# Kernel optimization log

Measured on AMD Instinct MI355X. Metric: run time of the kernel, lower is better.

The kernel has to match this reference:

```python
import jax, jax.numpy as jnp
import numpy as np

N = 50000   # nodes
E = 800000  # edges
H = 4       # num_heads
D = 32      # out_dim
IN = 256    # in_dim


def setup_inputs() -> dict:
    key = jax.random.key(0)
    k0, k1, k2, k3, k4, k5 = jax.random.split(key, 6)
    h = jax.random.normal(k0, (N, IN), dtype=jnp.float32)
    # fl weight (torch Linear stores [out, in]), xavier-ish scale
    Wl = jax.random.normal(k1, (H * D, IN), dtype=jnp.float32) * (1.0 / np.sqrt(IN))
    # fc / fq are initialized to small constants in torch; use small random here
    fc = jax.random.normal(k2, (IN, H * D), dtype=jnp.float32) * 0.02
    fq = jax.random.normal(k3, (IN, H * D), dtype=jnp.float32) * 0.02
    src = jax.random.randint(k4, (E,), 0, N)
    dst = jax.random.randint(k5, (E,), 0, N)
    return {"h": h, "Wl": Wl, "fc": fc, "fq": fq, "src": src, "dst": dst}


def reference(h, Wl, fc, fq, src, dst):
    n = h.shape[0]
    ft = (h @ Wl.T).reshape(n, H, D)      # [N,H,D]
    ft_c = (h @ fc).reshape(n, H, D)      # [N,H,D]
    ft_q = (h @ fq).reshape(n, H, D)      # [N,H,D]

    # edge attention: c = ft_c[dst], q = ft_q[src] - c, a = ELU(sum(q*c))
    c = ft_c[dst]                         # [E,H,D]
    a = jax.nn.elu(jnp.sum((ft_q[src] - c) * c, axis=-1))  # [E,H]

    # segmented (per-destination) softmax over incoming edges, per head
    m = jax.ops.segment_max(a, dst, num_segments=n)        # [N,H]
    ex = jnp.exp(a - m[dst])
    s = jax.ops.segment_sum(ex, dst, num_segments=n)       # [N,H]
    attn = ex / s[dst]                                     # [E,H]

    # global top-k (smallest l_s) threshold + mass redistribution, per head
    l_s = int(0.713 * attn.shape[0])
    srt = jnp.sort(attn, axis=0)                           # ascending per head
    thd = srt[l_s - 1]                                     # [H] l_s-th smallest
    topk_sum = jnp.sum(srt[:l_s], axis=0)                  # [H]
    a2 = jnp.where(attn - thd < 0, jnp.zeros((), attn.dtype), attn)
    ratio = (jnp.sum(a2, axis=0) + topk_sum) / jnp.sum(a2, axis=0)  # [H]
    a3 = a2 * ratio                                        # [E,H]

    # weighted scatter-sum of source features to destinations
    out = jax.ops.segment_sum(ft[src] * a3[:, :, None], dst, num_segments=n)  # [N,H,D]

    # concat=True: cat(flattened heads, mean over heads of ft)
    return jnp.concatenate([out.reshape(n, -1), ft.mean(axis=1)], axis=1)  # [N, H*D + D]
```

## Files before the change

kernel.cpp:

```cpp
#include <hip/hip_runtime.h>
#include <hip/hip_bf16.h>
#include <math.h>

#define N_NODES 50000
#define N_EDGES 800000
#define NH 4
#define DH 32
#define IN_DIM 256
#define OUTC 160
#define LS 570400
#define RANK0 (LS - 1)
#define DEG_CAP 160

typedef unsigned long long u64;
#define SC_FX 1099511627776.0

__global__ void k_deg(const int* __restrict__ dst, unsigned* __restrict__ A){
  int e = blockIdx.x * 256 + threadIdx.x;
  if (e < N_EDGES) atomicAdd(&A[dst[e]], 1u);
}

__global__ __launch_bounds__(1024) void k_scan(unsigned* __restrict__ A){
  __shared__ unsigned ps[1024];
  int t = threadIdx.x;
  const int CH = (N_NODES + 1023) / 1024;
  int base = t * CH;
  unsigned s = 0;
  for (int i = 0; i < CH; i++){ int n = base + i; if (n < N_NODES) s += A[n]; }
  ps[t] = s;
  __syncthreads();
  for (int off = 1; off < 1024; off <<= 1){
    unsigned v = (t >= off) ? ps[t - off] : 0;
    __syncthreads();
    ps[t] += v;
    __syncthreads();
  }
  unsigned ex = (t == 0) ? 0 : ps[t - 1];
  for (int i = 0; i < CH; i++){
    int n = base + i;
    if (n < N_NODES){ unsigned dv = A[n]; A[n] = ex; ex += dv; }
  }
}

__global__ void k_fill(const int* __restrict__ dst, unsigned* __restrict__ A,
                       unsigned* __restrict__ eidx){
  int e = blockIdx.x * 256 + threadIdx.x;
  if (e < N_EDGES) eidx[atomicAdd(&A[dst[e]], 1u)] = (unsigned)e;
}

__global__ void k_init(u64* __restrict__ sel4, unsigned* __restrict__ krem,
                       unsigned* __restrict__ cnt, unsigned* __restrict__ done,
                       unsigned* __restrict__ ccnt, u64* __restrict__ gsums){
  int t = threadIdx.x;
  if (t < 4){ sel4[t] = 0; krem[t] = RANK0; cnt[t] = 0; ccnt[t] = 0; }
  if (t < 8) gsums[t] = 0;
  if (t == 0) done[0] = 0;
}

#define BM 128
#define BK 16
__global__ __launch_bounds__(256) void k_gemm32(const float* __restrict__ A,
                                                const float* __restrict__ Wl,
                                                float* __restrict__ C){
  __shared__ float As[BK][BM + 4];
  __shared__ float Bs[BK][128 + 4];
  int tid = threadIdx.x;
  int m0 = blockIdx.x * BM;
  int ty = tid / 16, tx = tid % 16;
  float acc[8][8];
  #pragma unroll
  for (int i = 0; i < 8; i++)
    #pragma unroll
    for (int j = 0; j < 8; j++) acc[i][j] = 0.f;

  for (int k0 = 0; k0 < IN_DIM; k0 += BK){
    #pragma unroll
    for (int i = 0; i < 2; i++){
      int s = tid * 2 + i;
      int row = s >> 2, c4 = s & 3;
      int r = m0 + row;
      float4 v = make_float4(0.f, 0.f, 0.f, 0.f);
      if (r < N_NODES) v = *(const float4*)&A[(size_t)r * IN_DIM + k0 + c4 * 4];
      As[c4 * 4 + 0][row] = v.x; As[c4 * 4 + 1][row] = v.y;
      As[c4 * 4 + 2][row] = v.z; As[c4 * 4 + 3][row] = v.w;
    }
    #pragma unroll
    for (int i = 0; i < 2; i++){
      int s = tid * 2 + i;
      int j = s >> 2, c4 = s & 3;
      float4 v = *(const float4*)&Wl[(size_t)j * IN_DIM + k0 + c4 * 4];
      Bs[c4 * 4 + 0][j] = v.x; Bs[c4 * 4 + 1][j] = v.y;
      Bs[c4 * 4 + 2][j] = v.z; Bs[c4 * 4 + 3][j] = v.w;
    }
    __syncthreads();
    #pragma unroll
    for (int kk = 0; kk < BK; kk++){
      float4 a0 = *(const float4*)&As[kk][ty * 4];
      float4 a1 = *(const float4*)&As[kk][64 + ty * 4];
      float4 b0 = *(const float4*)&Bs[kk][tx * 4];
      float4 b1 = *(const float4*)&Bs[kk][64 + tx * 4];
      float av[8] = {a0.x, a0.y, a0.z, a0.w, a1.x, a1.y, a1.z, a1.w};
      float bv[8] = {b0.x, b0.y, b0.z, b0.w, b1.x, b1.y, b1.z, b1.w};
      #pragma unroll
      for (int i = 0; i < 8; i++)
        #pragma unroll
        for (int j = 0; j < 8; j++)
          acc[i][j] = fmaf(av[i], bv[j], acc[i][j]);
    }
    __syncthreads();
  }
  #pragma unroll
  for (int i = 0; i < 8; i++){
    int r = m0 + ((i < 4) ? (ty * 4 + i) : (64 + ty * 4 + (i - 4)));
    if (r >= N_NODES) continue;
    *(float4*)&C[(size_t)r * 128 + tx * 4]      = make_float4(acc[i][0], acc[i][1], acc[i][2], acc[i][3]);
    *(float4*)&C[(size_t)r * 128 + 64 + tx * 4] = make_float4(acc[i][4], acc[i][5], acc[i][6], acc[i][7]);
  }
}

__global__ __launch_bounds__(256) void k_gemm64(const float* __restrict__ A,
                                                const float* __restrict__ fc,
                                                const float* __restrict__ fq,
                                                double* __restrict__ c64,
                                                double* __restrict__ q64){
  __shared__ double As[16][66];
  __shared__ double Bs[16][66];
  int tid = threadIdx.x;
  int m0 = blockIdx.x * 64;
  int n0 = blockIdx.y * 64;
  const float* Bsrc = (n0 < 128) ? fc : fq;
  int j0 = (n0 < 128) ? n0 : n0 - 128;
  double* Cp = (n0 < 128) ? c64 : q64;
  int ty = tid / 16, tx = tid % 16;
  double acc[4][4];
  #pragma unroll
  for (int i = 0; i < 4; i++)
    #pragma unroll
    for (int j = 0; j < 4; j++) acc[i][j] = 0.0;

  for (int k0 = 0; k0 < IN_DIM; k0 += 16){
    {
      int row = tid >> 2, c4 = tid & 3;
      int r = m0 + row;
      float4 v = make_float4(0.f, 0.f, 0.f, 0.f);
      if (r < N_NODES) v = *(const float4*)&A[(size_t)r * IN_DIM + k0 + c4 * 4];
      As[c4 * 4 + 0][row] = (double)v.x; As[c4 * 4 + 1][row] = (double)v.y;
      As[c4 * 4 + 2][row] = (double)v.z; As[c4 * 4 + 3][row] = (double)v.w;
    }
    {
      int kr = tid >> 4, c4 = tid & 15;
      float4 v = *(const float4*)&Bsrc[(size_t)(k0 + kr) * 128 + j0 + c4 * 4];
      Bs[kr][c4 * 4 + 0] = (double)v.x; Bs[kr][c4 * 4 + 1] = (double)v.y;
      Bs[kr][c4 * 4 + 2] = (double)v.z; Bs[kr][c4 * 4 + 3] = (double)v.w;
    }
    __syncthreads();
    #pragma unroll
    for (int kk = 0; kk < 16; kk++){
      double a[4], b[4];
      #pragma unroll
      for (int i = 0; i < 4; i++) a[i] = As[kk][ty * 4 + i];
      #pragma unroll
      for (int j = 0; j < 4; j++) b[j] = Bs[kk][tx + 16 * j];
      #pragma unroll
      for (int i = 0; i < 4; i++)
        #pragma unroll
        for (int j = 0; j < 4; j++)
          acc[i][j] = fma(a[i], b[j], acc[i][j]);
    }
    __syncthreads();
  }
  #pragma unroll
  for (int i = 0; i < 4; i++){
    int r = m0 + ty * 4 + i;
    if (r >= N_NODES) continue;
    double* p = &Cp[(size_t)r * 128 + j0];
    #pragma unroll
    for (int j = 0; j < 4; j++) p[tx + 16 * j] = acc[i][j];
  }
}

__global__ __launch_bounds__(256) void k_softedge(const double* __restrict__ c64,
    const double* __restrict__ q64, const int* __restrict__ src,
    const unsigned* __restrict__ A, const unsigned* __restrict__ eidx,
    double* __restrict__ abuf){
  __shared__ double lds_a[4][DEG_CAP * 4];
  int d = blockIdx.x * 4 + (threadIdx.x >> 6);
  int t = threadIdx.x & 63;
  int wv = threadIdx.x >> 6;
  if (d >= N_NODES) return;
  unsigned k0 = d ? A[d - 1] : 0u, k1 = A[d];
  if (k0 == k1) return;
  double2 c = *(const double2*)&c64[(size_t)d * 128 + t * 2];
  double m = -1.0e300;
  int sn = src[eidx[k0]];
  double2 qn = *(const double2*)&q64[(size_t)sn * 128 + t * 2];
  for (unsigned k = k0; k < k1; k++){
    double2 q = qn;
    if (k + 1 < k1){
      int s2 = src[eidx[k + 1]];
      qn = *(const double2*)&q64[(size_t)s2 * 128 + t * 2];
    }
    double val = (q.x - c.x) * c.x + (q.y - c.y) * c.y;
    val += __shfl_xor(val, 1);
    val += __shfl_xor(val, 2);
    val += __shfl_xor(val, 4);
    val += __shfl_xor(val, 8);
    double a = (val > 0.0) ? val : expm1(val);
    m = fmax(m, a);
    if ((t & 15) == 0) lds_a[wv][(k - k0) * 4 + (t >> 4)] = a;
  }
  double mm = __shfl(m, (t & 3) * 16);
  unsigned nj = (k1 - k0) * 4;
  long long sfx = 0;
  for (unsigned jj = t; jj < nj; jj += 64){
    double ex = exp(lds_a[wv][jj] - mm);
    lds_a[wv][jj] = ex;
    sfx += llrint(ex * SC_FX);
  }
  #pragma unroll
  for (int msk = 4; msk < 64; msk <<= 1) sfx += __shfl_xor(sfx, msk);
  double sd = (double)sfx * (1.0 / SC_FX);
  for (unsigned jj = t; jj < nj; jj += 64)
    abuf[(size_t)k0 * 4 + jj] = lds_a[wv][jj] / sd;
}

__global__ __launch_bounds__(256) void k_hp(const double* __restrict__ attn,
    u64* __restrict__ sel4, unsigned* __restrict__ krem, unsigned* __restrict__ cnt,
    unsigned* __restrict__ hist, unsigned* __restrict__ done, u64 maskHi, int shift){
  __shared__ unsigned lh[1024];
  __shared__ unsigned ticket;
  for (int j = threadIdx.x; j < 1024; j += 256) lh[j] = 0;
  __syncthreads();
  int i0 = blockIdx.x * 256 + threadIdx.x;
  int hh = i0 & 3;
  u64 sel = sel4[hh] & maskHi;
  const int total = N_EDGES * 4;
  for (int i = i0; i < total; i += gridDim.x * 256){
    u64 u = (u64)__double_as_longlong(attn[i]);
    if ((u & maskHi) == sel)
      atomicAdd(&lh[hh * 256 + (unsigned)((u >> shift) & 255u)], 1u);
  }
  __syncthreads();
  for (int j = threadIdx.x; j < 1024; j += 256)
    if (lh[j]) atomicAdd(&hist[j], lh[j]);
  __threadfence();
  if (threadIdx.x == 0) ticket = atomicAdd(done, 1u);
  __syncthreads();
  if (ticket == gridDim.x - 1){
    __threadfence();
    for (int j = threadIdx.x; j < 1024; j += 256){ lh[j] = hist[j]; hist[j] = 0; }
    __syncthreads();
    if (threadIdx.x < 4){
      int t = threadIdx.x;
      unsigned kr = krem[t], cum = 0, b = 0;
      for (; b < 256; b++){
        unsigned c2 = lh[t * 256 + b];
        if (kr < cum + c2) break;
        cum += c2;
      }
      sel4[t] |= ((u64)b) << shift;
      krem[t] = kr - cum;
      cnt[t] += cum;
    }
    if (threadIdx.x == 0) *done = 0;
  }
}

__global__ __launch_bounds__(256) void k_compact(const double* __restrict__ attn,
    const u64* __restrict__ sel4, unsigned* __restrict__ ccnt,
    double* __restrict__ cand){
  __shared__ unsigned lcnt[4];
  __shared__ unsigned lbase[4];
  int t = threadIdx.x;
  if (t < 4) lcnt[t] = 0;
  __syncthreads();
  int i0 = blockIdx.x * 256 + t;
  int hh = i0 & 3;
  u64 sel = sel4[hh] & 0xFFFF000000000000ull;
  const int total = N_EDGES * 4;
  unsigned mc = 0;
  for (int i = i0; i < total; i += gridDim.x * 256){
    u64 u = (u64)__double_as_longlong(attn[i]);
    if ((u & 0xFFFF000000000000ull) == sel) mc++;
  }
  unsigned my_local = mc ? atomicAdd(&lcnt[hh], mc) : 0u;
  __syncthreads();
  if (t < 4) lbase[t] = lcnt[t] ? atomicAdd(&ccnt[t], lcnt[t]) : 0u;
  __syncthreads();
  if (mc == 0) return;
  unsigned pos = lbase[hh] + my_local;
  double* cp = cand + (size_t)hh * N_EDGES;
  for (int i = i0; i < total; i += gridDim.x * 256){
    double v = attn[i];
    u64 u = (u64)__double_as_longlong(v);
    if ((u & 0xFFFF000000000000ull) == sel) cp[pos++] = v;
  }
}

__global__ __launch_bounds__(256) void k_fin2(const double* __restrict__ cand,
    const unsigned* __restrict__ ccnt, u64* __restrict__ sel4,
    unsigned* __restrict__ krem, unsigned* __restrict__ cnt,
    unsigned* __restrict__ hist, unsigned* __restrict__ done, int shift){
  __shared__ unsigned lh[256];
  __shared__ unsigned ticket;
  int t = threadIdx.x;
  lh[t] = 0;
  __syncthreads();
  int h = blockIdx.x & 3;
  int bidx = blockIdx.x >> 2;
  int bph = gridDim.x >> 2;
  u64 maskHi = ~((1ull << (shift + 8)) - 1);
  u64 sel = sel4[h] & maskHi;
  unsigned n = ccnt[h];
  const double* cp = cand + (size_t)h * N_EDGES;
  for (unsigned i = bidx * 256 + t; i < n; i += bph * 256){
    u64 u = (u64)__double_as_longlong(cp[i]);
    if ((u & maskHi) == sel) atomicAdd(&lh[(unsigned)((u >> shift) & 255u)], 1u);
  }
  __syncthreads();
  if (lh[t]) atomicAdd(&hist[h * 256 + t], lh[t]);
  __threadfence();
  if (t == 0) ticket = atomicAdd(done, 1u);
  __syncthreads();
  if (ticket == gridDim.x - 1){
    __threadfence();
    __shared__ unsigned fh[1024];
    for (int j = t; j < 1024; j += 256){ fh[j] = hist[j]; hist[j] = 0; }
    __syncthreads();
    if (t < 4){
      unsigned kr = krem[t], cum = 0, b = 0;
      for (; b < 256; b++){
        unsigned c2 = fh[t * 256 + b];
        if (kr < cum + c2) break;
        cum += c2;
      }
      sel4[t] |= ((u64)b) << shift;
      krem[t] = kr - cum;
      cnt[t] += cum;
    }
    if (t == 0) *done = 0;
  }
}

__global__ __launch_bounds__(256) void k_sums(const double* __restrict__ attn,
    const u64* __restrict__ sel4, u64* __restrict__ gsums, float* __restrict__ a3){
  int t = threadIdx.x;
  int i0 = blockIdx.x * 256 + t;
  int hh = t & 3;
  double thd = __longlong_as_double((long long)sel4[hh]);
  double al = 0.0, ag = 0.0;
  const int total = N_EDGES * 4;
  for (int i = i0; i < total; i += gridDim.x * 256){
    double v = attn[i];
    if (v < thd){ al += v; a3[i] = 0.f; }
    else        { ag += v; a3[i] = (float)v; }
  }
  long long ql = llrint(al * SC_FX);
  long long qg = llrint(ag * SC_FX);
  #pragma unroll
  for (int m = 4; m < 64; m <<= 1){
    ql += __shfl_xor(ql, m);
    qg += __shfl_xor(qg, m);
  }
  __shared__ long long sl[16], sg[16];
  int wv = t >> 6;
  if ((t & 63) < 4){ sl[wv * 4 + hh] = ql; sg[wv * 4 + hh] = qg; }
  __syncthreads();
  if (t < 4){
    long long a = sl[t] + sl[4 + t] + sl[8 + t] + sl[12 + t];
    long long b = sg[t] + sg[4 + t] + sg[8 + t] + sg[12 + t];
    if (a) atomicAdd(&gsums[t],     (u64)a);
    if (b) atomicAdd(&gsums[4 + t], (u64)b);
  }
}

__global__ void k_ratio(const u64* __restrict__ sel4, const unsigned* __restrict__ cnt,
                        const u64* __restrict__ gsums, double* __restrict__ trd){
  int t = threadIdx.x;
  if (t < 4){
    double thd = __longlong_as_double((long long)sel4[t]);
    double sless = (double)gsums[t]     * (1.0 / SC_FX);
    double sge   = (double)gsums[4 + t] * (1.0 / SC_FX);
    double topk  = sless + (double)(LS - (int)cnt[t]) * thd;
    trd[t] = thd;
    trd[4 + t] = (sge + topk) / sge;
  }
}

__global__ __launch_bounds__(256) void k_scatter2(const float* __restrict__ ft,
    const int* __restrict__ src, const unsigned* __restrict__ A,
    const unsigned* __restrict__ eidx, const float* __restrict__ a3,
    const double* __restrict__ trd, float* __restrict__ out){
  int d = blockIdx.x * 4 + (threadIdx.x >> 6);
  int t = threadIdx.x & 63;
  if (d >= N_NODES) return;
  int hh = t >> 4;
  double ratio = trd[4 + hh];
  unsigned k0 = d ? A[d - 1] : 0u, k1 = A[d];
  long long acc0 = 0, acc1 = 0;
  float wn = (k0 < k1) ? a3[(size_t)k0 * 4 + hh] : 0.f;
  unsigned en = (k0 < k1) ? eidx[k0] : 0u;
  for (unsigned k = k0; k < k1; k++){
    float w = wn;
    unsigned e = en;
    if (k + 1 < k1){ wn = a3[(size_t)(k + 1) * 4 + hh]; en = eidx[k + 1]; }
    if (__ballot(w != 0.f) == 0ull) continue;
    if (w != 0.f){
      int s = src[e];
      float2 f = *(const float2*)&ft[(size_t)s * 128 + t * 2];
      double a3r = (double)w * ratio;
      acc0 += llrint(a3r * (double)f.x * SC_FX);
      acc1 += llrint(a3r * (double)f.y * SC_FX);
    }
  }
  float* p = &out[(size_t)d * OUTC + t * 2];
  p[0] = (float)((double)acc0 * (1.0 / SC_FX));
  p[1] = (float)((double)acc1 * (1.0 / SC_FX));
}

__global__ void k_mean(const float* __restrict__ ft, float* __restrict__ out){
  int i = blockIdx.x * 256 + threadIdx.x;
  if (i >= N_NODES * DH) return;
  int n = i / DH, dd = i % DH;
  const float* p = ft + (size_t)n * 128;
  out[(size_t)n * OUTC + 128 + dd] = 0.25f * (p[dd] + p[32 + dd] + p[64 + dd] + p[96 + dd]);
}

extern "C" void kernel_launch(void* const* d_in, const int* in_sizes, int n_in,
                              void* d_out, int out_size, void* d_ws, size_t ws_size,
                              hipStream_t stream){
  const float* h  = (const float*)d_in[0];
  const float* Wl = (const float*)d_in[1];
  const float* fc = (const float*)d_in[2];
  const float* fq = (const float*)d_in[3];
  const int* src  = (const int*)d_in[4];
  const int* dst  = (const int*)d_in[5];
  float* out = (float*)d_out;

  char* ws = (char*)d_ws;
  float*  ft32 = (float*)(ws);
  double* c64  = (double*)(ws + 25600000);
  float*  a3   = (float*)(ws + 25600000);
  double* q64  = (double*)(ws + 76800000);
  double* cand = (double*)(ws + 76800000);
  unsigned* A    = (unsigned*)(ws + 128000000);
  unsigned* eidx = (unsigned*)(ws + 128200064);
  unsigned* hist = (unsigned*)(ws + 131400064);
  u64*    sel4  = (u64*)(ws + 131404160);
  unsigned* krem = (unsigned*)(ws + 131404192);
  unsigned* cnt  = (unsigned*)(ws + 131404208);
  unsigned* done = (unsigned*)(ws + 131404224);
  unsigned* ccnt = (unsigned*)(ws + 131404240);
  u64*    gsums = (u64*)(ws + 131404256);
  double* trd   = (double*)(ws + 131404320);

  double* abuf = (double*)d_out;

  hipMemsetAsync(A, 0, 200004, stream);
  hipMemsetAsync(hist, 0, 4096, stream);
  k_init<<<1, 64, 0, stream>>>(sel4, krem, cnt, done, ccnt, gsums);

  k_deg<<<(N_EDGES + 255) / 256, 256, 0, stream>>>(dst, A);
  k_scan<<<1, 1024, 0, stream>>>(A);
  k_fill<<<(N_EDGES + 255) / 256, 256, 0, stream>>>(dst, A, eidx);

  k_gemm32<<<(N_NODES + BM - 1) / BM, 256, 0, stream>>>(h, Wl, ft32);
  dim3 g64((N_NODES + 63) / 64, 4);
  k_gemm64<<<g64, 256, 0, stream>>>(h, fc, fq, c64, q64);

  k_softedge<<<(N_NODES + 3) / 4, 256, 0, stream>>>(c64, q64, src, A, eidx, abuf);

  k_hp<<<1024, 256, 0, stream>>>(abuf, sel4, krem, cnt, hist, done, 0ull, 56);
  k_hp<<<1024, 256, 0, stream>>>(abuf, sel4, krem, cnt, hist, done,
                                 0xFF00000000000000ull, 48);
  k_compact<<<1024, 256, 0, stream>>>(abuf, sel4, ccnt, cand);
  for (int shift = 40; shift >= 0; shift -= 8)
    k_fin2<<<256, 256, 0, stream>>>(cand, ccnt, sel4, krem, cnt, hist, done, shift);

  k_sums<<<2048, 256, 0, stream>>>(abuf, sel4, gsums, a3);
  k_ratio<<<1, 64, 0, stream>>>(sel4, cnt, gsums, trd);

  k_scatter2<<<(N_NODES + 3) / 4, 256, 0, stream>>>(ft32, src, A, eidx, a3, trd, out);
  k_mean<<<(N_NODES * DH + 255) / 256, 256, 0, stream>>>(ft32, out);
}
```

Measured before the change: 1.051 ms.

## Switch attention pipeline to fp32 with fp64 refinement of near-threshold edges

Replaces the double-precision fc/fq GEMM and edge-softmax with fp32, fusing all three projections into one 384-column fp32 GEMM. The top-k radix select now works on 32-bit keys, which takes fewer histogram passes. Edges whose attention lies within a small relative margin of the threshold are collected and recomputed exactly in fp64 from the raw inputs, then reselected so the threshold and mass sums stay accurate. This halves memory traffic for the c/q tensors and avoids slow fp64 GEMM throughput. In exchange it adds extra passes and relies on the margin and the buffer capacity being large enough.

```diff
diff --git a/kernel.cpp b/kernel.cpp
--- a/kernel.cpp
+++ b/kernel.cpp
@@ -4,16 +4,18 @@
 
 #define N_NODES 50000
 #define N_EDGES 800000
-#define NH 4
 #define DH 32
 #define IN_DIM 256
 #define OUTC 160
 #define LS 570400
 #define RANK0 (LS - 1)
 #define DEG_CAP 160
+#define BCAP 65536
+#define MARG 3.0e-4
 
 typedef unsigned long long u64;
 #define SC_FX 1099511627776.0
+#define SC_32 4294967296.0
 
 __global__ void k_deg(const int* __restrict__ dst, unsigned* __restrict__ A){
   int e = blockIdx.x * 256 + threadIdx.x;
@@ -48,24 +50,27 @@
   if (e < N_EDGES) eidx[atomicAdd(&A[dst[e]], 1u)] = (unsigned)e;
 }
 
-__global__ void k_init(u64* __restrict__ sel4, unsigned* __restrict__ krem,
+__global__ void k_init(unsigned* __restrict__ sel32, unsigned* __restrict__ krem,
                        unsigned* __restrict__ cnt, unsigned* __restrict__ done,
-                       unsigned* __restrict__ ccnt, u64* __restrict__ gsums){
-  int t = threadIdx.x;
-  if (t < 4){ sel4[t] = 0; krem[t] = RANK0; cnt[t] = 0; ccnt[t] = 0; }
+                       unsigned* __restrict__ ccnt, unsigned* __restrict__ cbelow,
+                       unsigned* __restrict__ bcnt, unsigned* __restrict__ cntless,
+                       u64* __restrict__ gsums){
+  int t = threadIdx.x;
+  if (t < 4){ sel32[t]=0; krem[t]=RANK0; cnt[t]=0; ccnt[t]=0; cbelow[t]=0; cntless[t]=0; }
   if (t < 8) gsums[t] = 0;
-  if (t == 0) done[0] = 0;
+  if (t == 0){ done[0] = 0; bcnt[0] = 0; }
 }
 
 #define BM 128
 #define BK 16
-__global__ __launch_bounds__(256) void k_gemm32(const float* __restrict__ A,
-                                                const float* __restrict__ Wl,
-                                                float* __restrict__ C){
+__global__ __launch_bounds__(256) void k_gemm384(const float* __restrict__ A,
+    const float* __restrict__ Wl, const float* __restrict__ fc,
+    const float* __restrict__ fq, float* __restrict__ C){
   __shared__ float As[BK][BM + 4];
   __shared__ float Bs[BK][128 + 4];
   int tid = threadIdx.x;
   int m0 = blockIdx.x * BM;
+  int n0 = blockIdx.y * 128;
   int ty = tid / 16, tx = tid % 16;
   float acc[8][8];
   #pragma unroll
@@ -84,13 +89,23 @@
       As[c4 * 4 + 0][row] = v.x; As[c4 * 4 + 1][row] = v.y;
       As[c4 * 4 + 2][row] = v.z; As[c4 * 4 + 3][row] = v.w;
     }
-    #pragma unroll
-    for (int i = 0; i < 2; i++){
-      int s = tid * 2 + i;
-      int j = s >> 2, c4 = s & 3;
-      float4 v = *(const float4*)&Wl[(size_t)j * IN_DIM + k0 + c4 * 4];
-      Bs[c4 * 4 + 0][j] = v.x; Bs[c4 * 4 + 1][j] = v.y;
-      Bs[c4 * 4 + 2][j] = v.z; Bs[c4 * 4 + 3][j] = v.w;
+    if (n0 == 0){
+      #pragma unroll
+      for (int i = 0; i < 2; i++){
+        int s = tid * 2 + i;
+        int j = s >> 2, c4 = s & 3;
+        float4 v = *(const float4*)&Wl[(size_t)j * IN_DIM + k0 + c4 * 4];
+        Bs[c4 * 4 + 0][j] = v.x; Bs[c4 * 4 + 1][j] = v.y;
+        Bs[c4 * 4 + 2][j] = v.z; Bs[c4 * 4 + 3][j] = v.w;
+      }
+    } else {
+      const float* Bsrc = (n0 == 128) ? fc : fq;
+      #pragma unroll
+      for (int i = 0; i < 2; i++){
+        int s = tid * 2 + i;
+        int kr = s >> 5, c4 = s & 31;
+        *(float4*)&Bs[kr][c4 * 4] = *(const float4*)&Bsrc[(size_t)(k0 + kr) * 128 + c4 * 4];
+      }
     }
     __syncthreads();
     #pragma unroll
@@ -113,132 +128,70 @@
   for (int i = 0; i < 8; i++){
     int r = m0 + ((i < 4) ? (ty * 4 + i) : (64 + ty * 4 + (i - 4)));
     if (r >= N_NODES) continue;
-    *(float4*)&C[(size_t)r * 128 + tx * 4]      = make_float4(acc[i][0], acc[i][1], acc[i][2], acc[i][3]);
-    *(float4*)&C[(size_t)r * 128 + 64 + tx * 4] = make_float4(acc[i][4], acc[i][5], acc[i][6], acc[i][7]);
-  }
-}
-
-__global__ __launch_bounds__(256) void k_gemm64(const float* __restrict__ A,
-                                                const float* __restrict__ fc,
-                                                const float* __restrict__ fq,
-                                                double* __restrict__ c64,
-                                                double* __restrict__ q64){
-  __shared__ double As[16][66];
-  __shared__ double Bs[16][66];
-  int tid = threadIdx.x;
-  int m0 = blockIdx.x * 64;
-  int n0 = blockIdx.y * 64;
-  const float* Bsrc = (n0 < 128) ? fc : fq;
-  int j0 = (n0 < 128) ? n0 : n0 - 128;
-  double* Cp = (n0 < 128) ? c64 : q64;
-  int ty = tid / 16, tx = tid % 16;
-  double acc[4][4];
-  #pragma unroll
-  for (int i = 0; i < 4; i++)
-    #pragma unroll
-    for (int j = 0; j < 4; j++) acc[i][j] = 0.0;
-
-  for (int k0 = 0; k0 < IN_DIM; k0 += 16){
-    {
-      int row = tid >> 2, c4 = tid & 3;
-      int r = m0 + row;
-      float4 v = make_float4(0.f, 0.f, 0.f, 0.f);
-      if (r < N_NODES) v = *(const float4*)&A[(size_t)r * IN_DIM + k0 + c4 * 4];
-      As[c4 * 4 + 0][row] = (double)v.x; As[c4 * 4 + 1][row] = (double)v.y;
-      As[c4 * 4 + 2][row] = (double)v.z; As[c4 * 4 + 3][row] = (double)v.w;
-    }
-    {
-      int kr = tid >> 4, c4 = tid & 15;
-      float4 v = *(const float4*)&Bsrc[(size_t)(k0 + kr) * 128 + j0 + c4 * 4];
-      Bs[kr][c4 * 4 + 0] = (double)v.x; Bs[kr][c4 * 4 + 1] = (double)v.y;
-      Bs[kr][c4 * 4 + 2] = (double)v.z; Bs[kr][c4 * 4 + 3] = (double)v.w;
-    }
-    __syncthreads();
-    #pragma unroll
-    for (int kk = 0; kk < 16; kk++){
-      double a[4], b[4];
-      #pragma unroll
-      for (int i = 0; i < 4; i++) a[i] = As[kk][ty * 4 + i];
-      #pragma unroll
-      for (int j = 0; j < 4; j++) b[j] = Bs[kk][tx + 16 * j];
-      #pragma unroll
-      for (int i = 0; i < 4; i++)
-        #pragma unroll
-        for (int j = 0; j < 4; j++)
-          acc[i][j] = fma(a[i], b[j], acc[i][j]);
-    }
-    __syncthreads();
-  }
-  #pragma unroll
-  for (int i = 0; i < 4; i++){
-    int r = m0 + ty * 4 + i;
-    if (r >= N_NODES) continue;
-    double* p = &Cp[(size_t)r * 128 + j0];
-    #pragma unroll
-    for (int j = 0; j < 4; j++) p[tx + 16 * j] = acc[i][j];
-  }
-}
-
-__global__ __launch_bounds__(256) void k_softedge(const double* __restrict__ c64,
-    const double* __restrict__ q64, const int* __restrict__ src,
-    const unsigned* __restrict__ A, const unsigned* __restrict__ eidx,
-    double* __restrict__ abuf){
-  __shared__ double lds_a[4][DEG_CAP * 4];
+    *(float4*)&C[(size_t)r * 384 + n0 + tx * 4]      = make_float4(acc[i][0], acc[i][1], acc[i][2], acc[i][3]);
+    *(float4*)&C[(size_t)r * 384 + n0 + 64 + tx * 4] = make_float4(acc[i][4], acc[i][5], acc[i][6], acc[i][7]);
+  }
+}
+
+__global__ __launch_bounds__(256) void k_softedge32(const float* __restrict__ fcq,
+    const int* __restrict__ src, const unsigned* __restrict__ A,
+    const unsigned* __restrict__ eidx, float* __restrict__ abuf){
+  __shared__ float lds_a[4][DEG_CAP * 4];
   int d = blockIdx.x * 4 + (threadIdx.x >> 6);
   int t = threadIdx.x & 63;
   int wv = threadIdx.x >> 6;
   if (d >= N_NODES) return;
   unsigned k0 = d ? A[d - 1] : 0u, k1 = A[d];
   if (k0 == k1) return;
-  double2 c = *(const double2*)&c64[(size_t)d * 128 + t * 2];
-  double m = -1.0e300;
+  float2 c = *(const float2*)&fcq[(size_t)d * 384 + 128 + t * 2];
+  float m = -1.0e30f;
   int sn = src[eidx[k0]];
-  double2 qn = *(const double2*)&q64[(size_t)sn * 128 + t * 2];
+  float2 qn = *(const float2*)&fcq[(size_t)sn * 384 + 256 + t * 2];
   for (unsigned k = k0; k < k1; k++){
-    double2 q = qn;
+    float2 q = qn;
     if (k + 1 < k1){
       int s2 = src[eidx[k + 1]];
-      qn = *(const double2*)&q64[(size_t)s2 * 128 + t * 2];
-    }
-    double val = (q.x - c.x) * c.x + (q.y - c.y) * c.y;
+      qn = *(const float2*)&fcq[(size_t)s2 * 384 + 256 + t * 2];
+    }
+    float val = (q.x - c.x) * c.x + (q.y - c.y) * c.y;
     val += __shfl_xor(val, 1);
     val += __shfl_xor(val, 2);
     val += __shfl_xor(val, 4);
     val += __shfl_xor(val, 8);
-    double a = (val > 0.0) ? val : expm1(val);
-    m = fmax(m, a);
+    float a = (val > 0.f) ? val : expm1f(val);
+    m = fmaxf(m, a);
     if ((t & 15) == 0) lds_a[wv][(k - k0) * 4 + (t >> 4)] = a;
   }
-  double mm = __shfl(m, (t & 3) * 16);
+  float mm = __shfl(m, (t & 3) * 16);
   unsigned nj = (k1 - k0) * 4;
   long long sfx = 0;
   for (unsigned jj = t; jj < nj; jj += 64){
-    double ex = exp(lds_a[wv][jj] - mm);
+    float ex = __expf(lds_a[wv][jj] - mm);
     lds_a[wv][jj] = ex;
-    sfx += llrint(ex * SC_FX);
+    sfx += (long long)llrintf(ex * (float)SC_32);
   }
   #pragma unroll
   for (int msk = 4; msk < 64; msk <<= 1) sfx += __shfl_xor(sfx, msk);
-  double sd = (double)sfx * (1.0 / SC_FX);
+  float sd = (float)((double)sfx * (1.0 / SC_32));
   for (unsigned jj = t; jj < nj; jj += 64)
     abuf[(size_t)k0 * 4 + jj] = lds_a[wv][jj] / sd;
 }
 
-__global__ __launch_bounds__(256) void k_hp(const double* __restrict__ attn,
-    u64* __restrict__ sel4, unsigned* __restrict__ krem, unsigned* __restrict__ cnt,
-    unsigned* __restrict__ hist, unsigned* __restrict__ done, u64 maskHi, int shift){
+__global__ __launch_bounds__(256) void k_hp32(const float* __restrict__ attn,
+    unsigned* __restrict__ sel32, unsigned* __restrict__ krem, unsigned* __restrict__ cnt,
+    unsigned* __restrict__ hist, unsigned* __restrict__ done, unsigned maskHi, int shift){
   __shared__ unsigned lh[1024];
   __shared__ unsigned ticket;
   for (int j = threadIdx.x; j < 1024; j += 256) lh[j] = 0;
   __syncthreads();
   int i0 = blockIdx.x * 256 + threadIdx.x;
   int hh = i0 & 3;
-  u64 sel = sel4[hh] & maskHi;
+  unsigned sel = sel32[hh] & maskHi;
   const int total = N_EDGES * 4;
   for (int i = i0; i < total; i += gridDim.x * 256){
-    u64 u = (u64)__double_as_longlong(attn[i]);
+    unsigned u = __float_as_uint(attn[i]);
     if ((u & maskHi) == sel)
-      atomicAdd(&lh[hh * 256 + (unsigned)((u >> shift) & 255u)], 1u);
+      atomicAdd(&lh[hh * 256 + ((u >> shift) & 255u)], 1u);
   }
   __syncthreads();
   for (int j = threadIdx.x; j < 1024; j += 256)
@@ -258,7 +211,7 @@
         if (kr < cum + c2) break;
         cum += c2;
       }
-      sel4[t] |= ((u64)b) << shift;
+      sel32[t] |= b << shift;
       krem[t] = kr - cum;
       cnt[t] += cum;
     }
@@ -266,9 +219,9 @@
   }
 }
 
-__global__ __launch_bounds__(256) void k_compact(const double* __restrict__ attn,
-    const u64* __restrict__ sel4, unsigned* __restrict__ ccnt,
-    double* __restrict__ cand){
+__global__ __launch_bounds__(256) void k_compact32(const float* __restrict__ attn,
+    const unsigned* __restrict__ sel32, unsigned* __restrict__ ccnt,
+    float* __restrict__ cand){
   __shared__ unsigned lcnt[4];
   __shared__ unsigned lbase[4];
   int t = threadIdx.x;
@@ -276,12 +229,12 @@
   __syncthreads();
   int i0 = blockIdx.x * 256 + t;
   int hh = i0 & 3;
-  u64 sel = sel4[hh] & 0xFFFF000000000000ull;
+  unsigned sel = sel32[hh] & 0xFFFF0000u;
   const int total = N_EDGES * 4;
   unsigned mc = 0;
   for (int i = i0; i < total; i += gridDim.x * 256){
-    u64 u = (u64)__double_as_longlong(attn[i]);
-    if ((u & 0xFFFF000000000000ull) == sel) mc++;
+    unsigned u = __float_as_uint(attn[i]);
+    if ((u & 0xFFFF0000u) == sel) mc++;
   }
   unsigned my_local = mc ? atomicAdd(&lcnt[hh], mc) : 0u;
   __syncthreads();
@@ -289,16 +242,16 @@
   __syncthreads();
   if (mc == 0) return;
   unsigned pos = lbase[hh] + my_local;
-  double* cp = cand + (size_t)hh * N_EDGES;
+  float* cp = cand + (size_t)hh * N_EDGES;
   for (int i = i0; i < total; i += gridDim.x * 256){
-    double v = attn[i];
-    u64 u = (u64)__double_as_longlong(v);
-    if ((u & 0xFFFF000000000000ull) == sel) cp[pos++] = v;
-  }
-}
-
-__global__ __launch_bounds__(256) void k_fin2(const double* __restrict__ cand,
-    const unsigned* __restrict__ ccnt, u64* __restrict__ sel4,
+    float v = attn[i];
+    unsigned u = __float_as_uint(v);
+    if ((u & 0xFFFF0000u) == sel) cp[pos++] = v;
+  }
+}
+
+__global__ __launch_bounds__(256) void k_fin32(const float* __restrict__ cand,
+    const unsigned* __restrict__ ccnt, unsigned* __restrict__ sel32,
     unsigned* __restrict__ krem, unsigned* __restrict__ cnt,
     unsigned* __restrict__ hist, unsigned* __restrict__ done, int shift){
   __shared__ unsigned lh[256];
@@ -309,13 +262,13 @@
   int h = blockIdx.x & 3;
   int bidx = blockIdx.x >> 2;
   int bph = gridDim.x >> 2;
-  u64 maskHi = ~((1ull << (shift + 8)) - 1);
-  u64 sel = sel4[h] & maskHi;
+  unsigned maskHi = ~((1u << (shift + 8)) - 1u);
+  unsigned sel = sel32[h] & maskHi;
   unsigned n = ccnt[h];
-  const double* cp = cand + (size_t)h * N_EDGES;
+  const float* cp = cand + (size_t)h * N_EDGES;
   for (unsigned i = bidx * 256 + t; i < n; i += bph * 256){
-    u64 u = (u64)__double_as_longlong(cp[i]);
-    if ((u & maskHi) == sel) atomicAdd(&lh[(unsigned)((u >> shift) & 255u)], 1u);
+    unsigned u = __float_as_uint(cp[i]);
+    if ((u & maskHi) == sel) atomicAdd(&lh[(u >> shift) & 255u], 1u);
   }
   __syncthreads();
   if (lh[t]) atomicAdd(&hist[h * 256 + t], lh[t]);
@@ -334,7 +287,7 @@
         if (kr < cum + c2) break;
         cum += c2;
       }
-      sel4[t] |= ((u64)b) << shift;
+      sel32[t] |= b << shift;
       krem[t] = kr - cum;
       cnt[t] += cum;
     }
@@ -342,18 +295,155 @@
   }
 }
 
-__global__ __launch_bounds__(256) void k_sums(const double* __restrict__ attn,
-    const u64* __restrict__ sel4, u64* __restrict__ gsums, float* __restrict__ a3){
+__global__ __launch_bounds__(256) void k_bmark(const float* __restrict__ attn,
+    const unsigned* __restrict__ sel32, unsigned* __restrict__ cbelow,
+    unsigned* __restrict__ bcnt, unsigned* __restrict__ blist){
   int t = threadIdx.x;
   int i0 = blockIdx.x * 256 + t;
   int hh = t & 3;
-  double thd = __longlong_as_double((long long)sel4[hh]);
+  double thd = (double)__uint_as_float(sel32[hh]);
+  double lo = thd * (1.0 - MARG), hi = thd * (1.0 + MARG);
+  unsigned below = 0;
+  const int total = N_EDGES * 4;
+  for (int i = i0; i < total; i += gridDim.x * 256){
+    double v = (double)attn[i];
+    if (v < lo) below++;
+    else if (v <= hi){
+      unsigned p = atomicAdd(bcnt, 1u);
+      if (p < BCAP) blist[p] = (unsigned)i;
+    }
+  }
+  #pragma unroll
+  for (int m = 4; m < 64; m <<= 1) below += __shfl_xor(below, m);
+  __shared__ unsigned sb[16];
+  int wv = t >> 6;
+  if ((t & 63) < 4) sb[wv * 4 + hh] = below;
+  __syncthreads();
+  if (t < 4){
+    unsigned b = sb[t] + sb[4 + t] + sb[8 + t] + sb[12 + t];
+    if (b) atomicAdd(&cbelow[t], b);
+  }
+}
+
+__global__ __launch_bounds__(256) void k_brefine(const float* __restrict__ h,
+    const float* __restrict__ fc, const float* __restrict__ fq,
+    const int* __restrict__ src, const int* __restrict__ dst,
+    const unsigned* __restrict__ A, const unsigned* __restrict__ eidx,
+    const unsigned* __restrict__ blist, const unsigned* __restrict__ bcnt,
+    double* __restrict__ bval){
+  __shared__ double la[4][DEG_CAP];
+  int wv = threadIdx.x >> 6;
+  int l = threadIdx.x & 63;
+  int j = l & 31;
+  unsigned nb = *bcnt; if (nb > BCAP) nb = BCAP;
+  for (unsigned idx = blockIdx.x * 4 + wv; idx < nb; idx += gridDim.x * 4){
+    unsigned slot = blist[idx];
+    unsigned kslot = slot >> 2;
+    int hh = slot & 3;
+    int d = dst[eidx[kslot]];
+    unsigned k0 = d ? A[d - 1] : 0u, k1 = A[d];
+    int col = hh * 32 + j;
+    const float* hd = h + (size_t)d * 256;
+    double c = 0.0;
+    for (int i = 0; i < 256; i += 4){
+      float4 hv = *(const float4*)&hd[i];
+      c = fma((double)hv.x, (double)fc[(size_t)(i + 0) * 128 + col], c);
+      c = fma((double)hv.y, (double)fc[(size_t)(i + 1) * 128 + col], c);
+      c = fma((double)hv.z, (double)fc[(size_t)(i + 2) * 128 + col], c);
+      c = fma((double)hv.w, (double)fc[(size_t)(i + 3) * 128 + col], c);
+    }
+    double m = -1.0e300, atgt = 0.0;
+    for (unsigned k = k0; k < k1; k++){
+      int s = src[eidx[k]];
+      const float* hs = h + (size_t)s * 256;
+      double q = 0.0;
+      for (int i = 0; i < 256; i += 4){
+        float4 hv = *(const float4*)&hs[i];
+        q = fma((double)hv.x, (double)fq[(size_t)(i + 0) * 128 + col], q);
+        q = fma((double)hv.y, (double)fq[(size_t)(i + 1) * 128 + col], q);
+        q = fma((double)hv.z, (double)fq[(size_t)(i + 2) * 128 + col], q);
+        q = fma((double)hv.w, (double)fq[(size_t)(i + 3) * 128 + col], q);
+      }
+      double p = (q - c) * c;
+      p += __shfl_xor(p, 1);
+      p += __shfl_xor(p, 2);
+      p += __shfl_xor(p, 4);
+      p += __shfl_xor(p, 8);
+      p += __shfl_xor(p, 16);
+      double a = (p > 0.0) ? p : expm1(p);
+      m = fmax(m, a);
+      if (l == 0) la[wv][k - k0] = a;
+      if (k == kslot) atgt = a;
+    }
+    long long sfx = 0;
+    for (unsigned kk = l; kk < k1 - k0; kk += 64)
+      sfx += llrint(exp(la[wv][kk] - m) * SC_FX);
+    #pragma unroll
+    for (int msk = 1; msk < 64; msk <<= 1) sfx += __shfl_xor(sfx, msk);
+    double sd = (double)sfx * (1.0 / SC_FX);
+    if (l == 0) bval[idx] = exp(atgt - m) / sd;
+  }
+}
+
+__global__ __launch_bounds__(256) void k_bselect(const double* __restrict__ bval,
+    const unsigned* __restrict__ blist, const unsigned* __restrict__ bcnt,
+    const unsigned* __restrict__ cbelow, double* __restrict__ thd64,
+    unsigned* __restrict__ cntless){
+  __shared__ unsigned lh[256];
+  __shared__ u64 s_sel;
+  __shared__ unsigned s_kr, s_cnt;
+  int hsel = blockIdx.x;
+  int t = threadIdx.x;
+  unsigned nb = *bcnt; if (nb > BCAP) nb = BCAP;
+  if (t == 0){ s_sel = 0; s_kr = RANK0 - cbelow[hsel]; s_cnt = 0; }
+  __syncthreads();
+  for (int p = 0; p < 8; p++){
+    int shift = 56 - 8 * p;
+    u64 maskHi = (p == 0) ? 0ull : (~0ull) << (64 - 8 * p);
+    lh[t] = 0;
+    __syncthreads();
+    u64 sel = s_sel;
+    for (unsigned i = t; i < nb; i += 256){
+      if ((int)(blist[i] & 3) == hsel){
+        u64 u = (u64)__double_as_longlong(bval[i]);
+        if ((u & maskHi) == sel) atomicAdd(&lh[(unsigned)((u >> shift) & 255u)], 1u);
+      }
+    }
+    __syncthreads();
+    if (t == 0){
+      unsigned kr = s_kr, cum = 0, b = 0;
+      for (; b < 256; b++){
+        unsigned c2 = lh[b];
+        if (kr < cum + c2) break;
+        cum += c2;
+      }
+      s_sel |= ((u64)b) << shift;
+      s_kr = kr - cum;
+      s_cnt += cum;
+    }
+    __syncthreads();
+  }
+  if (t == 0){
+    thd64[hsel] = __longlong_as_double((long long)s_sel);
+    cntless[hsel] = cbelow[hsel] + s_cnt;
+  }
+}
+
+__global__ __launch_bounds__(256) void k_sums32(const float* __restrict__ attn,
+    const unsigned* __restrict__ sel32, u64* __restrict__ gsums, float* __restrict__ a3){
+  int t = threadIdx.x;
+  int i0 = blockIdx.x * 256 + t;
+  int hh = t & 3;
+  double thd = (double)__uint_as_float(sel32[hh]);
+  double lo = thd * (1.0 - MARG), hi = thd * (1.0 + MARG);
   double al = 0.0, ag = 0.0;
   const int total = N_EDGES * 4;
   for (int i = i0; i < total; i += gridDim.x * 256){
-    double v = attn[i];
-    if (v < thd){ al += v; a3[i] = 0.f; }
-    else        { ag += v; a3[i] = (float)v; }
+    float vf = attn[i];
+    double v = (double)vf;
+    if (v < lo){ al += v; a3[i] = 0.f; }
+    else if (v > hi){ ag += v; a3[i] = vf; }
+    else a3[i] = 0.f;
   }
   long long ql = llrint(al * SC_FX);
   long long qg = llrint(ag * SC_FX);
@@ -374,20 +464,33 @@
   }
 }
 
-__global__ void k_ratio(const u64* __restrict__ sel4, const unsigned* __restrict__ cnt,
+__global__ void k_bfinal(const unsigned* __restrict__ blist, const double* __restrict__ bval,
+    const unsigned* __restrict__ bcnt, const double* __restrict__ thd64,
+    u64* __restrict__ gsums, float* __restrict__ a3){
+  unsigned nb = *bcnt; if (nb > BCAP) nb = BCAP;
+  for (unsigned idx = blockIdx.x * 256 + threadIdx.x; idx < nb; idx += gridDim.x * 256){
+    unsigned slot = blist[idx];
+    int hh = slot & 3;
+    double v = bval[idx];
+    bool kept = (v >= thd64[hh]);
+    a3[slot] = kept ? (float)v : 0.f;
+    atomicAdd(&gsums[(kept ? 4 : 0) + hh], (u64)llrint(v * SC_FX));
+  }
+}
+
+__global__ void k_ratio(const double* __restrict__ thd64, const unsigned* __restrict__ cntless,
                         const u64* __restrict__ gsums, double* __restrict__ trd){
   int t = threadIdx.x;
   if (t < 4){
-    double thd = __longlong_as_double((long long)sel4[t]);
-    double sless = (double)gsums[t]     * (1.0 / SC_FX);
-    double sge   = (double)gsums[4 + t] * (1.0 / SC_FX);
-    double topk  = sless + (double)(LS - (int)cnt[t]) * thd;
-    trd[t] = thd;
+    double sless = (double)(long long)gsums[t]     * (1.0 / SC_FX);
+    double sge   = (double)(long long)gsums[4 + t] * (1.0 / SC_FX);
+    double topk  = sless + (double)(LS - (int)cntless[t]) * thd64[t];
+    trd[t] = thd64[t];
     trd[4 + t] = (sge + topk) / sge;
   }
 }
 
-__global__ __launch_bounds__(256) void k_scatter2(const float* __restrict__ ft,
+__global__ __launch_bounds__(256) void k_scatter2(const float* __restrict__ fcq,
     const int* __restrict__ src, const unsigned* __restrict__ A,
     const unsigned* __restrict__ eidx, const float* __restrict__ a3,
     const double* __restrict__ trd, float* __restrict__ out){
@@ -407,7 +510,7 @@
     if (__ballot(w != 0.f) == 0ull) continue;
     if (w != 0.f){
       int s = src[e];
-      float2 f = *(const float2*)&ft[(size_t)s * 128 + t * 2];
+      float2 f = *(const float2*)&fcq[(size_t)s * 384 + t * 2];
       double a3r = (double)w * ratio;
       acc0 += llrint(a3r * (double)f.x * SC_FX);
       acc1 += llrint(a3r * (double)f.y * SC_FX);
@@ -418,11 +521,11 @@
   p[1] = (float)((double)acc1 * (1.0 / SC_FX));
 }
 
-__global__ void k_mean(const float* __restrict__ ft, float* __restrict__ out){
+__global__ void k_mean(const float* __restrict__ fcq, float* __restrict__ out){
   int i = blockIdx.x * 256 + threadIdx.x;
   if (i >= N_NODES * DH) return;
   int n = i / DH, dd = i % DH;
-  const float* p = ft + (size_t)n * 128;
+  const float* p = fcq + (size_t)n * 384;
   out[(size_t)n * OUTC + 128 + dd] = 0.25f * (p[dd] + p[32 + dd] + p[64 + dd] + p[96 + dd]);
 }
 
@@ -438,48 +541,55 @@
   float* out = (float*)d_out;
 
   char* ws = (char*)d_ws;
-  float*  ft32 = (float*)(ws);
-  double* c64  = (double*)(ws + 25600000);
-  float*  a3   = (float*)(ws + 25600000);
-  double* q64  = (double*)(ws + 76800000);
-  double* cand = (double*)(ws + 76800000);
-  unsigned* A    = (unsigned*)(ws + 128000000);
-  unsigned* eidx = (unsigned*)(ws + 128200064);
-  unsigned* hist = (unsigned*)(ws + 131400064);
-  u64*    sel4  = (u64*)(ws + 131404160);
-  unsigned* krem = (unsigned*)(ws + 131404192);
-  unsigned* cnt  = (unsigned*)(ws + 131404208);
-  unsigned* done = (unsigned*)(ws + 131404224);
-  unsigned* ccnt = (unsigned*)(ws + 131404240);
-  u64*    gsums = (u64*)(ws + 131404256);
-  double* trd   = (double*)(ws + 131404320);
-
-  double* abuf = (double*)d_out;
+  float*    fcq  = (float*)(ws);
+  unsigned* A    = (unsigned*)(ws + 76800000);
+  unsigned* eidx = (unsigned*)(ws + 77000064);
+  float*    a3   = (float*)(ws + 80200064);
+  unsigned* hist = (unsigned*)(ws + 93000064);
+  unsigned* sel32  = (unsigned*)(ws + 93004160);
+  unsigned* krem   = (unsigned*)(ws + 93004176);
+  unsigned* cnt    = (unsigned*)(ws + 93004192);
+  unsigned* done   = (unsigned*)(ws + 93004208);
+  unsigned* ccnt   = (unsigned*)(ws + 93004224);
+  unsigned* cbelow = (unsigned*)(ws + 93004240);
+  unsigned* bcnt   = (unsigned*)(ws + 93004256);
+  unsigned* cntless= (unsigned*)(ws + 93004272);
+  u64*      gsums  = (u64*)(ws + 93004288);
+  double*   thd64  = (double*)(ws + 93004352);
+  double*   trd    = (double*)(ws + 93004416);
+  unsigned* blist  = (unsigned*)(ws + 93008896);
+  double*   bval   = (double*)(ws + 93271040);
+
+  float* abuf = (float*)d_out;
+  float* cand = (float*)((char*)d_out + 12800000);
 
   hipMemsetAsync(A, 0, 200004, stream);
   hipMemsetAsync(hist, 0, 4096, stream);
-  k_init<<<1, 64, 0, stream>>>(sel4, krem, cnt, done, ccnt, gsums);
+  k_init<<<1, 64, 0, stream>>>(sel32, krem, cnt, done, ccnt, cbelow, bcnt, cntless, gsums);
 
   k_deg<<<(N_EDGES + 255) / 256, 256, 0, stream>>>(dst, A);
   k_scan<<<1, 1024, 0, stream>>>(A);
   k_fill<<<(N_EDGES + 255) / 256, 256, 0, stream>>>(dst, A, eidx);
 
-  k_gemm32<<<(N_NODES + BM - 1) / BM, 256, 0, stream>>>(h, Wl, ft32);
-  dim3 g64((N_NODES + 63) / 64, 4);
-  k_gemm64<<<g64, 256, 0, stream>>>(h, fc, fq, c64, q64);
-
-  k_softedge<<<(N_NODES + 3) / 4, 256, 0, stream>>>(c64, q64, src, A, eidx, abuf);
-
-  k_hp<<<1024, 256, 0, stream>>>(abuf, sel4, krem, cnt, hist, done, 0ull, 56);
-  k_hp<<<1024, 256, 0, stream>>>(abuf, sel4, krem, cnt, hist, done,
-                                 0xFF00000000000000ull, 48);
-  k_compact<<<1024, 256, 0, stream>>>(abuf, sel4, ccnt, cand);
-  for (int shift = 40; shift >= 0; shift -= 8)
-    k_fin2<<<256, 256, 0, stream>>>(cand, ccnt, sel4, krem, cnt, hist, done, shift);
-
-  k_sums<<<2048, 256, 0, stream>>>(abuf, sel4, gsums, a3);
-  k_ratio<<<1, 64, 0, stream>>>(sel4, cnt, gsums, trd);
-
-  k_scatter2<<<(N_NODES + 3) / 4, 256, 0, stream>>>(ft32, src, A, eidx, a3, trd, out);
-  k_mean<<<(N_NODES * DH + 255) / 256, 256, 0, stream>>>(ft32, out);
-}
+  dim3 gg((N_NODES + BM - 1) / BM, 3);
+  k_gemm384<<<gg, 256, 0, stream>>>(h, Wl, fc, fq, fcq);
+
+  k_softedge32<<<(N_NODES + 3) / 4, 256, 0, stream>>>(fcq, src, A, eidx, abuf);
+
+  k_hp32<<<1024, 256, 0, stream>>>(abuf, sel32, krem, cnt, hist, done, 0u, 24);
+  k_hp32<<<1024, 256, 0, stream>>>(abuf, sel32, krem, cnt, hist, done, 0xFF000000u, 16);
+  k_compact32<<<1024, 256, 0, stream>>>(abuf, sel32, ccnt, cand);
+  k_fin32<<<256, 256, 0, stream>>>(cand, ccnt, sel32, krem, cnt, hist, done, 8);
+  k_fin32<<<256, 256, 0, stream>>>(cand, ccnt, sel32, krem, cnt, hist, done, 0);
+
+  k_bmark<<<1024, 256, 0, stream>>>(abuf, sel32, cbelow, bcnt, blist);
+  k_brefine<<<512, 256, 0, stream>>>(h, fc, fq, src, dst, A, eidx, blist, bcnt, bval);
+  k_bselect<<<4, 256, 0, stream>>>(bval, blist, bcnt, cbelow, thd64, cntless);
+
+  k_sums32<<<2048, 256, 0, stream>>>(abuf, sel32, gsums, a3);
+  k_bfinal<<<64, 256, 0, stream>>>(blist, bval, bcnt, thd64, gsums, a3);
+  k_ratio<<<1, 64, 0, stream>>>(thd64, cntless, gsums, trd);
+
+  k_scatter2<<<(N_NODES + 3) / 4, 256, 0, stream>>>(fcq, src, A, eidx, a3, trd, out);
+  k_mean<<<(N_NODES * DH + 255) / 256, 256, 0, stream>>>(fcq, out);
+}
```

New measurement: 1.562 ms. 1.49x slower.
